# Kernel optimization log

Hardware: AMD Instinct MI355X
Metric: run time of the kernel (lower is better)

Reference implementation:

```python
import jax, jax.numpy as jnp
import numpy as np

DIM_IN, DIM_Q, DIM_K = 1024, 128, 128
B, S = 8, 2048

def setup_inputs() -> dict:
    key = jax.random.key(0)
    ks = jax.random.split(key, 9)
    sq = 1.0 / np.sqrt(DIM_IN)
    return {
        "query": jax.random.normal(ks[0], (B, S, DIM_IN), jnp.float32),
        "key": jax.random.normal(ks[1], (B, S, DIM_IN), jnp.float32),
        "value": jax.random.normal(ks[2], (B, S, DIM_IN), jnp.float32),
        "Wq": jax.random.uniform(ks[3], (DIM_IN, DIM_Q), jnp.float32, -sq, sq),
        "bq": jax.random.uniform(ks[4], (DIM_Q,), jnp.float32, -sq, sq),
        "Wk": jax.random.uniform(ks[5], (DIM_IN, DIM_K), jnp.float32, -sq, sq),
        "bk": jax.random.uniform(ks[6], (DIM_K,), jnp.float32, -sq, sq),
        "Wv": jax.random.uniform(ks[7], (DIM_IN, DIM_K), jnp.float32, -sq, sq),
        "bv": jax.random.uniform(ks[8], (DIM_K,), jnp.float32, -sq, sq),
    }

def reference(query, key, value, Wq, bq, Wk, bk, Wv, bv):
    q = jnp.einsum("bsd,dq->bsq", query, Wq) + bq          # [B,S,Dq]
    k = jnp.einsum("bsd,dk->bsk", key, Wk) + bk            # [B,S,Dk]
    v = jnp.einsum("bsd,dk->bsk", value, Wv) + bv          # [B,S,Dk]
    scale = jnp.asarray(q.shape[-1] ** 0.5, q.dtype)
    scores = jnp.einsum("bqd,bkd->bqk", q, k) / scale      # [B,S,S]
    attn = jax.nn.softmax(scores, axis=-1)
    return jnp.einsum("bqk,bkd->bqd", attn, v)             # [B,S,Dk]
```

## Files before the change

### kernel.cpp

```cpp
#include <hip/hip_runtime.h>

typedef __attribute__((ext_vector_type(8))) short short8;
typedef __attribute__((ext_vector_type(4))) float floatx4;

#define MFMA16(a, b, c) __builtin_amdgcn_mfma_f32_16x16x32_bf16(a, b, c, 0, 0, 0)

__device__ __forceinline__ short f2bf(float f) {
    unsigned int u = __float_as_uint(f);
    u = u + 0x7fffu + ((u >> 16) & 1u);
    return (short)(u >> 16);
}

__device__ __forceinline__ void ldst16(const void* g, void* l) {
    __builtin_amdgcn_global_load_lds(
        (const __attribute__((address_space(1))) void*)g,
        (__attribute__((address_space(3))) void*)l, 16, 0, 0);
}

__global__ __launch_bounds__(256) void wconv_kernel(const float* __restrict__ Wq,
                                                    const float* __restrict__ Wk,
                                                    const float* __restrict__ Wv,
                                                    short* __restrict__ wt) {
    int idx = blockIdx.x * 256 + threadIdx.x;
    int w = idx >> 17;
    int rem = idx & 131071;
    int k = rem >> 7, n = rem & 127;
    const float* W = (w == 0) ? Wq : (w == 1) ? Wk : Wv;
    wt[w * 131072 + n * 1024 + k] = f2bf(W[rem]);
}

__global__ __launch_bounds__(128, 3) void proj_kernel(const float* __restrict__ Q,
                                                      const float* __restrict__ K,
                                                      const float* __restrict__ V,
                                                      const short* __restrict__ wt,
                                                      const float* __restrict__ bq,
                                                      const float* __restrict__ bk,
                                                      const float* __restrict__ bv,
                                                      short* __restrict__ qo,
                                                      short* __restrict__ ko,
                                                      short* __restrict__ vo) {
    alignas(16) __shared__ float Asl[32 * 64];
    alignas(16) __shared__ short Wsl[128 * 64];
    const int t = threadIdx.x;
    const int wv = t >> 6, L = t & 63;
    const int q4 = L >> 4, l16 = L & 15;
    const int which = blockIdx.y;
    const float* A = (which == 0) ? Q : (which == 1) ? K : V;
    const short* Wt = wt + which * 131072;
    const float* bias = (which == 0) ? bq : (which == 1) ? bk : bv;
    const int m0 = blockIdx.x * 32;
    const int mw = m0 + 16 * wv;

    floatx4 acc[8];
    for (int nt = 0; nt < 8; nt++) acc[nt] = (floatx4)0.0f;

    for (int k0 = 0; k0 < 1024; k0 += 64) {
        __syncthreads();
        for (int j = 0; j < 4; j++) {
            int s = j * 128 + t;
            int r = s >> 4, c = (s & 15) ^ (r & 15);
            ldst16(A + (size_t)(m0 + r) * 1024 + k0 + c * 4,
                   Asl + (j * 128 + 64 * wv) * 4);
        }
        for (int j = 0; j < 8; j++) {
            int s = j * 128 + t;
            int r = s >> 3, c = (s & 7) ^ (r & 7);
            ldst16(Wt + (size_t)r * 1024 + k0 + c * 8,
                   Wsl + (j * 128 + 64 * wv) * 8);
        }
        __syncthreads();

        for (int ks = 0; ks < 2; ks++) {
            int c0 = 8 * ks + 2 * q4;
            const int ar = 16 * wv + l16;
            float4 f0 = *(float4*)&Asl[ar * 64 + (c0 ^ l16) * 4];
            float4 f1 = *(float4*)&Asl[ar * 64 + ((c0 + 1) ^ l16) * 4];
            short8 af;
            af[0] = f2bf(f0.x); af[1] = f2bf(f0.y); af[2] = f2bf(f0.z); af[3] = f2bf(f0.w);
            af[4] = f2bf(f1.x); af[5] = f2bf(f1.y); af[6] = f2bf(f1.z); af[7] = f2bf(f1.w);
            int cw = 4 * ks + q4;
            for (int nt = 0; nt < 8; nt++) {
                int wr = 16 * nt + l16;
                short8 bf = *(short8*)&Wsl[wr * 64 + (cw ^ (l16 & 7)) * 8];
                acc[nt] = MFMA16(af, bf, acc[nt]);
            }
        }
    }

    for (int nt = 0; nt < 8; nt++) {
        float bvv = bias[16 * nt + l16];
        for (int r = 0; r < 4; r++) {
            float val = acc[nt][r] + bvv;
            short h = f2bf(val);
            int grow = mw + q4 * 4 + r;
            int col = 16 * nt + l16;
            if (which == 0) {
                qo[(size_t)grow * 128 + col] = h;
            } else if (which == 1) {
                ko[(size_t)grow * 128 + col] = h;
            } else {
                int bb = grow >> 11, s = grow & 2047;
                vo[(size_t)bb * 262144 + (size_t)col * 2048 + s] = h;
            }
        }
    }
}

__global__ __launch_bounds__(512, 2) void flash_kernel(const short* __restrict__ qw,
                                                       const short* __restrict__ kw,
                                                       const short* __restrict__ vw,
                                                       float* __restrict__ out) {
    alignas(16) __shared__ short Kls[2][64 * 128];
    alignas(16) __shared__ short Vls[2][128 * 64];
    alignas(16) __shared__ short Pl[2][64][72];
    const int t = threadIdx.x;
    const int wvi = t >> 6, L = t & 63;
    const int pr = wvi >> 2, wq = wvi & 3;
    const int pt = t & 255;
    const int q4 = L >> 4, l16 = L & 15;
    const int bq = blockIdx.x, b = blockIdx.y;
    const short* qp = qw + (size_t)b * 262144 + (size_t)bq * 64 * 128;
    const short* kp = kw + (size_t)b * 262144;
    const short* vp = vw + (size_t)b * 262144;

    short8 qf[4];
    for (int ks = 0; ks < 4; ks++)
        qf[ks] = *(const short8*)(qp + (16 * wq + l16) * 128 + ks * 32 + q4 * 8);

    floatx4 oacc[8];
    for (int dt = 0; dt < 8; dt++) oacc[dt] = (floatx4)0.0f;
    float ps[4] = {0.f, 0.f, 0.f, 0.f};
    const float SL = (float)(0.08838834764831845 * 1.4426950408889634);

    for (int kt = 0; kt < 16; kt++) {
        const int kv0 = pr * 1024 + kt * 64;
        __syncthreads();
        for (int j = 0; j < 4; j++) {
            int s = j * 256 + pt;
            int r = s >> 4, c = (s & 15) ^ (r & 15);
            ldst16(kp + (size_t)(kv0 + r) * 128 + c * 8,
                   &Kls[pr][(j * 256 + 64 * wq) * 8]);
        }
        for (int j = 0; j < 4; j++) {
            int s = j * 256 + pt;
            int r = s >> 3, c = (s & 7) ^ (r & 7);
            ldst16(vp + (size_t)r * 2048 + kv0 + c * 8,
                   &Vls[pr][(j * 256 + 64 * wq) * 8]);
        }
        __syncthreads();

        floatx4 sa[4];
        for (int nt = 0; nt < 4; nt++) {
            sa[nt] = (floatx4)0.0f;
            for (int ks = 0; ks < 4; ks++) {
                short8 bfr = *(short8*)&Kls[pr][(16 * nt + l16) * 128 + ((4 * ks + q4) ^ l16) * 8];
                sa[nt] = MFMA16(qf[ks], bfr, sa[nt]);
            }
        }

        for (int nt = 0; nt < 4; nt++) {
            for (int r = 0; r < 4; r++) {
                float pv = __builtin_amdgcn_exp2f(sa[nt][r] * SL - 4.0f);
                ps[r] += pv;
                Pl[pr][16 * wq + q4 * 4 + r][16 * nt + l16] = f2bf(pv);
            }
        }

        short8 pf0 = *(short8*)&Pl[pr][16 * wq + l16][q4 * 8];
        short8 pf1 = *(short8*)&Pl[pr][16 * wq + l16][32 + q4 * 8];
        for (int dt = 0; dt < 8; dt++) {
            short8 v0 = *(short8*)&Vls[pr][(16 * dt + l16) * 64 + (q4 ^ (l16 & 7)) * 8];
            short8 v1 = *(short8*)&Vls[pr][(16 * dt + l16) * 64 + ((4 + q4) ^ (l16 & 7)) * 8];
            oacc[dt] = MFMA16(pf0, v0, oacc[dt]);
            oacc[dt] = MFMA16(pf1, v1, oacc[dt]);
        }
    }

    for (int r = 0; r < 4; r++)
        for (int off = 1; off <= 8; off <<= 1)
            ps[r] += __shfl_xor(ps[r], off, 64);

    __syncthreads();
    float* Om = (float*)&Kls[0][0];
    float* Lm = (float*)&Vls[0][0];
    if (pr == 1) {
        for (int dt = 0; dt < 8; dt++)
            for (int r = 0; r < 4; r++)
                Om[(16 * wq + q4 * 4 + r) * 128 + 16 * dt + l16] = oacc[dt][r];
        if (l16 == 0)
            for (int r = 0; r < 4; r++)
                Lm[16 * wq + q4 * 4 + r] = ps[r];
    }
    __syncthreads();
    if (pr == 0) {
        float inv[4];
        for (int r = 0; r < 4; r++)
            inv[r] = 1.0f / (ps[r] + Lm[16 * wq + q4 * 4 + r]);
        for (int dt = 0; dt < 8; dt++) {
            for (int r = 0; r < 4; r++) {
                int row = 16 * wq + q4 * 4 + r;
                int qrow = bq * 64 + row;
                out[((size_t)b * 2048 + qrow) * 128 + 16 * dt + l16] =
                    (oacc[dt][r] + Om[row * 128 + 16 * dt + l16]) * inv[r];
            }
        }
    }
}

extern "C" void kernel_launch(void* const* d_in, const int* in_sizes, int n_in,
                              void* d_out, int out_size, void* d_ws, size_t ws_size,
                              hipStream_t stream) {
    const float* query = (const float*)d_in[0];
    const float* key   = (const float*)d_in[1];
    const float* value = (const float*)d_in[2];
    const float* Wq    = (const float*)d_in[3];
    const float* bq    = (const float*)d_in[4];
    const float* Wk    = (const float*)d_in[5];
    const float* bk    = (const float*)d_in[6];
    const float* Wv    = (const float*)d_in[7];
    const float* bv    = (const float*)d_in[8];
    float* out = (float*)d_out;

    short* wt  = (short*)d_ws;
    short* qws = wt + 3 * 131072;
    short* kws = qws + 16384 * 128;
    short* vws = kws + 16384 * 128;

    wconv_kernel<<<1536, 256, 0, stream>>>(Wq, Wk, Wv, wt);
    proj_kernel<<<dim3(512, 3), 128, 0, stream>>>(query, key, value, wt,
                                                  bq, bk, bv, qws, kws, vws);
    flash_kernel<<<dim3(32, 8), 512, 0, stream>>>(qws, kws, vws, out);
}
```

Baseline: 271.3 us.

## Drop LDS staging in projection; load A and W directly into registers with prefetch

```diff
diff --git a/kernel.cpp b/kernel.cpp
--- a/kernel.cpp
+++ b/kernel.cpp
@@ -29,18 +29,16 @@
     wt[w * 131072 + n * 1024 + k] = f2bf(W[rem]);
 }
 
-__global__ __launch_bounds__(128, 3) void proj_kernel(const float* __restrict__ Q,
-                                                      const float* __restrict__ K,
-                                                      const float* __restrict__ V,
-                                                      const short* __restrict__ wt,
-                                                      const float* __restrict__ bq,
-                                                      const float* __restrict__ bk,
-                                                      const float* __restrict__ bv,
-                                                      short* __restrict__ qo,
-                                                      short* __restrict__ ko,
-                                                      short* __restrict__ vo) {
-    alignas(16) __shared__ float Asl[32 * 64];
-    alignas(16) __shared__ short Wsl[128 * 64];
+__global__ __launch_bounds__(128) void proj_kernel(const float* __restrict__ Q,
+                                                   const float* __restrict__ K,
+                                                   const float* __restrict__ V,
+                                                   const short* __restrict__ wt,
+                                                   const float* __restrict__ bq,
+                                                   const float* __restrict__ bk,
+                                                   const float* __restrict__ bv,
+                                                   short* __restrict__ qo,
+                                                   short* __restrict__ ko,
+                                                   short* __restrict__ vo) {
     const int t = threadIdx.x;
     const int wv = t >> 6, L = t & 63;
     const int q4 = L >> 4, l16 = L & 15;
@@ -48,59 +46,81 @@
     const float* A = (which == 0) ? Q : (which == 1) ? K : V;
     const short* Wt = wt + which * 131072;
     const float* bias = (which == 0) ? bq : (which == 1) ? bk : bv;
-    const int m0 = blockIdx.x * 32;
-    const int mw = m0 + 16 * wv;
-
-    floatx4 acc[8];
-    for (int nt = 0; nt < 8; nt++) acc[nt] = (floatx4)0.0f;
+    const int m0 = blockIdx.x * 64 + wv * 32;
+
+    floatx4 acc[2][8];
+#pragma unroll
+    for (int rg = 0; rg < 2; rg++)
+#pragma unroll
+        for (int nt = 0; nt < 8; nt++) acc[rg][nt] = (floatx4)0.0f;
+
+    const float* a0 = A + (size_t)(m0 + l16) * 1024 + 8 * q4;
+    const float* a1 = a0 + 16 * 1024;
+    const short* wb = Wt + (size_t)l16 * 1024 + 8 * q4;
+
+    float4 pa[2][2][2];
+#pragma unroll
+    for (int rg = 0; rg < 2; rg++) {
+        const float* ap = rg ? a1 : a0;
+#pragma unroll
+        for (int ks = 0; ks < 2; ks++) {
+            pa[rg][ks][0] = *(const float4*)(ap + 32 * ks);
+            pa[rg][ks][1] = *(const float4*)(ap + 32 * ks + 4);
+        }
+    }
 
     for (int k0 = 0; k0 < 1024; k0 += 64) {
-        __syncthreads();
-        for (int j = 0; j < 4; j++) {
-            int s = j * 128 + t;
-            int r = s >> 4, c = (s & 15) ^ (r & 15);
-            ldst16(A + (size_t)(m0 + r) * 1024 + k0 + c * 4,
-                   Asl + (j * 128 + 64 * wv) * 4);
-        }
-        for (int j = 0; j < 8; j++) {
-            int s = j * 128 + t;
-            int r = s >> 3, c = (s & 7) ^ (r & 7);
-            ldst16(Wt + (size_t)r * 1024 + k0 + c * 8,
-                   Wsl + (j * 128 + 64 * wv) * 8);
-        }
-        __syncthreads();
-
-        for (int ks = 0; ks < 2; ks++) {
-            int c0 = 8 * ks + 2 * q4;
-            const int ar = 16 * wv + l16;
-            float4 f0 = *(float4*)&Asl[ar * 64 + (c0 ^ l16) * 4];
-            float4 f1 = *(float4*)&Asl[ar * 64 + ((c0 + 1) ^ l16) * 4];
-            short8 af;
-            af[0] = f2bf(f0.x); af[1] = f2bf(f0.y); af[2] = f2bf(f0.z); af[3] = f2bf(f0.w);
-            af[4] = f2bf(f1.x); af[5] = f2bf(f1.y); af[6] = f2bf(f1.z); af[7] = f2bf(f1.w);
-            int cw = 4 * ks + q4;
+        short8 af[2][2];
+#pragma unroll
+        for (int rg = 0; rg < 2; rg++)
+#pragma unroll
+            for (int ks = 0; ks < 2; ks++) {
+                float4 f0 = pa[rg][ks][0], f1 = pa[rg][ks][1];
+                short8 v;
+                v[0] = f2bf(f0.x); v[1] = f2bf(f0.y); v[2] = f2bf(f0.z); v[3] = f2bf(f0.w);
+                v[4] = f2bf(f1.x); v[5] = f2bf(f1.y); v[6] = f2bf(f1.z); v[7] = f2bf(f1.w);
+                af[rg][ks] = v;
+            }
+        if (k0 + 64 < 1024) {
+#pragma unroll
+            for (int rg = 0; rg < 2; rg++) {
+                const float* ap = (rg ? a1 : a0) + k0 + 64;
+#pragma unroll
+                for (int ks = 0; ks < 2; ks++) {
+                    pa[rg][ks][0] = *(const float4*)(ap + 32 * ks);
+                    pa[rg][ks][1] = *(const float4*)(ap + 32 * ks + 4);
+                }
+            }
+        }
+#pragma unroll
+        for (int ks = 0; ks < 2; ks++)
+#pragma unroll
             for (int nt = 0; nt < 8; nt++) {
-                int wr = 16 * nt + l16;
-                short8 bf = *(short8*)&Wsl[wr * 64 + (cw ^ (l16 & 7)) * 8];
-                acc[nt] = MFMA16(af, bf, acc[nt]);
-            }
-        }
-    }
-
-    for (int nt = 0; nt < 8; nt++) {
-        float bvv = bias[16 * nt + l16];
-        for (int r = 0; r < 4; r++) {
-            float val = acc[nt][r] + bvv;
-            short h = f2bf(val);
-            int grow = mw + q4 * 4 + r;
-            int col = 16 * nt + l16;
-            if (which == 0) {
-                qo[(size_t)grow * 128 + col] = h;
-            } else if (which == 1) {
-                ko[(size_t)grow * 128 + col] = h;
-            } else {
-                int bb = grow >> 11, s = grow & 2047;
-                vo[(size_t)bb * 262144 + (size_t)col * 2048 + s] = h;
+                short8 bf = *(const short8*)(wb + (size_t)nt * 16384 + k0 + 32 * ks);
+                acc[0][nt] = MFMA16(af[0][ks], bf, acc[0][nt]);
+                acc[1][nt] = MFMA16(af[1][ks], bf, acc[1][nt]);
+            }
+    }
+
+#pragma unroll
+    for (int rg = 0; rg < 2; rg++) {
+        const int rbase = m0 + rg * 16 + q4 * 4;
+#pragma unroll
+        for (int nt = 0; nt < 8; nt++) {
+            const int col = 16 * nt + l16;
+            float bvv = bias[col];
+#pragma unroll
+            for (int r = 0; r < 4; r++) {
+                short h = f2bf(acc[rg][nt][r] + bvv);
+                int grow = rbase + r;
+                if (which == 0) {
+                    qo[(size_t)grow * 128 + col] = h;
+                } else if (which == 1) {
+                    ko[(size_t)grow * 128 + col] = h;
+                } else {
+                    int bb = grow >> 11, s = grow & 2047;
+                    vo[(size_t)bb * 262144 + (size_t)col * 2048 + s] = h;
+                }
             }
         }
     }
@@ -227,7 +247,7 @@
     short* vws = kws + 16384 * 128;
 
     wconv_kernel<<<1536, 256, 0, stream>>>(Wq, Wk, Wv, wt);
-    proj_kernel<<<dim3(512, 3), 128, 0, stream>>>(query, key, value, wt,
+    proj_kernel<<<dim3(256, 3), 128, 0, stream>>>(query, key, value, wt,
                                                   bq, bk, bv, qws, kws, vws);
     flash_kernel<<<dim3(32, 8), 512, 0, stream>>>(qws, kws, vws, out);
 }
```

After: 282.0 us. 4.0% more time.

## Register-prefetch projection without LDS and double-buffer K/V tiles in flash kernel

Applied to the files above, without the earlier changes.

```diff
diff --git a/kernel.cpp b/kernel.cpp
--- a/kernel.cpp
+++ b/kernel.cpp
@@ -29,7 +29,36 @@
     wt[w * 131072 + n * 1024 + k] = f2bf(W[rem]);
 }
 
-__global__ __launch_bounds__(128, 3) void proj_kernel(const float* __restrict__ Q,
+#define CONV8(dst, f0, f1)                                                  \
+    {                                                                       \
+        dst[0] = f2bf(f0.x); dst[1] = f2bf(f0.y);                           \
+        dst[2] = f2bf(f0.z); dst[3] = f2bf(f0.w);                           \
+        dst[4] = f2bf(f1.x); dst[5] = f2bf(f1.y);                           \
+        dst[6] = f2bf(f1.z); dst[7] = f2bf(f1.w);                           \
+    }
+
+#define SUBSTEP(P0, P1, P2, P3, cc)                                         \
+    {                                                                       \
+        short8 af0, af1;                                                    \
+        CONV8(af0, P0, P1);                                                 \
+        CONV8(af1, P2, P3);                                                 \
+        if ((cc) + 2 < 16) {                                                \
+            const float* ap = aP + ((cc) + 2) * 64;                         \
+            P0 = *(const float4*)(ap);                                      \
+            P1 = *(const float4*)(ap + 4);                                  \
+            P2 = *(const float4*)(ap + 32);                                 \
+            P3 = *(const float4*)(ap + 36);                                 \
+        }                                                                   \
+        _Pragma("unroll")                                                   \
+        for (int nt = 0; nt < 4; nt++) {                                    \
+            short8 b0 = *(const short8*)(wP + nt * 16384 + (cc) * 64);      \
+            short8 b1 = *(const short8*)(wP + nt * 16384 + (cc) * 64 + 32); \
+            acc[nt] = MFMA16(af0, b0, acc[nt]);                             \
+            acc[nt] = MFMA16(af1, b1, acc[nt]);                             \
+        }                                                                   \
+    }
+
+__global__ __launch_bounds__(128, 4) void proj_kernel(const float* __restrict__ Q,
                                                       const float* __restrict__ K,
                                                       const float* __restrict__ V,
                                                       const short* __restrict__ wt,
@@ -39,8 +68,6 @@
                                                       short* __restrict__ qo,
                                                       short* __restrict__ ko,
                                                       short* __restrict__ vo) {
-    alignas(16) __shared__ float Asl[32 * 64];
-    alignas(16) __shared__ short Wsl[128 * 64];
     const int t = threadIdx.x;
     const int wv = t >> 6, L = t & 63;
     const int q4 = L >> 4, l16 = L & 15;
@@ -48,52 +75,39 @@
     const float* A = (which == 0) ? Q : (which == 1) ? K : V;
     const short* Wt = wt + which * 131072;
     const float* bias = (which == 0) ? bq : (which == 1) ? bk : bv;
-    const int m0 = blockIdx.x * 32;
-    const int mw = m0 + 16 * wv;
-
-    floatx4 acc[8];
-    for (int nt = 0; nt < 8; nt++) acc[nt] = (floatx4)0.0f;
-
-    for (int k0 = 0; k0 < 1024; k0 += 64) {
-        __syncthreads();
-        for (int j = 0; j < 4; j++) {
-            int s = j * 128 + t;
-            int r = s >> 4, c = (s & 15) ^ (r & 15);
-            ldst16(A + (size_t)(m0 + r) * 1024 + k0 + c * 4,
-                   Asl + (j * 128 + 64 * wv) * 4);
-        }
-        for (int j = 0; j < 8; j++) {
-            int s = j * 128 + t;
-            int r = s >> 3, c = (s & 7) ^ (r & 7);
-            ldst16(Wt + (size_t)r * 1024 + k0 + c * 8,
-                   Wsl + (j * 128 + 64 * wv) * 8);
-        }
-        __syncthreads();
-
-        for (int ks = 0; ks < 2; ks++) {
-            int c0 = 8 * ks + 2 * q4;
-            const int ar = 16 * wv + l16;
-            float4 f0 = *(float4*)&Asl[ar * 64 + (c0 ^ l16) * 4];
-            float4 f1 = *(float4*)&Asl[ar * 64 + ((c0 + 1) ^ l16) * 4];
-            short8 af;
-            af[0] = f2bf(f0.x); af[1] = f2bf(f0.y); af[2] = f2bf(f0.z); af[3] = f2bf(f0.w);
-            af[4] = f2bf(f1.x); af[5] = f2bf(f1.y); af[6] = f2bf(f1.z); af[7] = f2bf(f1.w);
-            int cw = 4 * ks + q4;
-            for (int nt = 0; nt < 8; nt++) {
-                int wr = 16 * nt + l16;
-                short8 bf = *(short8*)&Wsl[wr * 64 + (cw ^ (l16 & 7)) * 8];
-                acc[nt] = MFMA16(af, bf, acc[nt]);
-            }
-        }
-    }
-
-    for (int nt = 0; nt < 8; nt++) {
-        float bvv = bias[16 * nt + l16];
+    const int m0 = blockIdx.x * 16;
+    const int n0 = wv * 64;
+
+    floatx4 acc[4];
+#pragma unroll
+    for (int nt = 0; nt < 4; nt++) acc[nt] = (floatx4)0.0f;
+
+    const float* aP = A + (size_t)(m0 + l16) * 1024 + 8 * q4;
+    const short* wP = Wt + (size_t)(n0 + l16) * 1024 + 8 * q4;
+
+    float4 pA0 = *(const float4*)(aP);
+    float4 pA1 = *(const float4*)(aP + 4);
+    float4 pA2 = *(const float4*)(aP + 32);
+    float4 pA3 = *(const float4*)(aP + 36);
+    float4 pB0 = *(const float4*)(aP + 64);
+    float4 pB1 = *(const float4*)(aP + 68);
+    float4 pB2 = *(const float4*)(aP + 96);
+    float4 pB3 = *(const float4*)(aP + 100);
+
+    for (int c = 0; c < 16; c += 2) {
+        SUBSTEP(pA0, pA1, pA2, pA3, c);
+        SUBSTEP(pB0, pB1, pB2, pB3, c + 1);
+    }
+
+    const int rbase = m0 + q4 * 4;
+#pragma unroll
+    for (int nt = 0; nt < 4; nt++) {
+        const int col = n0 + 16 * nt + l16;
+        float bvv = bias[col];
+#pragma unroll
         for (int r = 0; r < 4; r++) {
-            float val = acc[nt][r] + bvv;
-            short h = f2bf(val);
-            int grow = mw + q4 * 4 + r;
-            int col = 16 * nt + l16;
+            short h = f2bf(acc[nt][r] + bvv);
+            int grow = rbase + r;
             if (which == 0) {
                 qo[(size_t)grow * 128 + col] = h;
             } else if (which == 1) {
@@ -110,8 +124,8 @@
                                                        const short* __restrict__ kw,
                                                        const short* __restrict__ vw,
                                                        float* __restrict__ out) {
-    alignas(16) __shared__ short Kls[2][64 * 128];
-    alignas(16) __shared__ short Vls[2][128 * 64];
+    alignas(16) __shared__ short Kls[2][2][64 * 128];
+    alignas(16) __shared__ short Vls[2][2][128 * 64];
     alignas(16) __shared__ short Pl[2][64][72];
     const int t = threadIdx.x;
     const int wvi = t >> 6, L = t & 63;
@@ -132,28 +146,34 @@
     float ps[4] = {0.f, 0.f, 0.f, 0.f};
     const float SL = (float)(0.08838834764831845 * 1.4426950408889634);
 
-    for (int kt = 0; kt < 16; kt++) {
+    auto stage = [&](int buf, int kt) {
         const int kv0 = pr * 1024 + kt * 64;
-        __syncthreads();
         for (int j = 0; j < 4; j++) {
             int s = j * 256 + pt;
             int r = s >> 4, c = (s & 15) ^ (r & 15);
             ldst16(kp + (size_t)(kv0 + r) * 128 + c * 8,
-                   &Kls[pr][(j * 256 + 64 * wq) * 8]);
+                   &Kls[buf][pr][(j * 256 + 64 * wq) * 8]);
         }
         for (int j = 0; j < 4; j++) {
             int s = j * 256 + pt;
             int r = s >> 3, c = (s & 7) ^ (r & 7);
             ldst16(vp + (size_t)r * 2048 + kv0 + c * 8,
-                   &Vls[pr][(j * 256 + 64 * wq) * 8]);
-        }
+                   &Vls[buf][pr][(j * 256 + 64 * wq) * 8]);
+        }
+    };
+
+    stage(0, 0);
+
+    for (int kt = 0; kt < 16; kt++) {
+        const int cur = kt & 1;
         __syncthreads();
+        if (kt + 1 < 16) stage(cur ^ 1, kt + 1);
 
         floatx4 sa[4];
         for (int nt = 0; nt < 4; nt++) {
             sa[nt] = (floatx4)0.0f;
             for (int ks = 0; ks < 4; ks++) {
-                short8 bfr = *(short8*)&Kls[pr][(16 * nt + l16) * 128 + ((4 * ks + q4) ^ l16) * 8];
+                short8 bfr = *(short8*)&Kls[cur][pr][(16 * nt + l16) * 128 + ((4 * ks + q4) ^ l16) * 8];
                 sa[nt] = MFMA16(qf[ks], bfr, sa[nt]);
             }
         }
@@ -169,8 +189,8 @@
         short8 pf0 = *(short8*)&Pl[pr][16 * wq + l16][q4 * 8];
         short8 pf1 = *(short8*)&Pl[pr][16 * wq + l16][32 + q4 * 8];
         for (int dt = 0; dt < 8; dt++) {
-            short8 v0 = *(short8*)&Vls[pr][(16 * dt + l16) * 64 + (q4 ^ (l16 & 7)) * 8];
-            short8 v1 = *(short8*)&Vls[pr][(16 * dt + l16) * 64 + ((4 + q4) ^ (l16 & 7)) * 8];
+            short8 v0 = *(short8*)&Vls[cur][pr][(16 * dt + l16) * 64 + (q4 ^ (l16 & 7)) * 8];
+            short8 v1 = *(short8*)&Vls[cur][pr][(16 * dt + l16) * 64 + ((4 + q4) ^ (l16 & 7)) * 8];
             oacc[dt] = MFMA16(pf0, v0, oacc[dt]);
             oacc[dt] = MFMA16(pf1, v1, oacc[dt]);
         }
@@ -181,8 +201,8 @@
             ps[r] += __shfl_xor(ps[r], off, 64);
 
     __syncthreads();
-    float* Om = (float*)&Kls[0][0];
-    float* Lm = (float*)&Vls[0][0];
+    float* Om = (float*)&Kls[0][0][0];
+    float* Lm = (float*)&Vls[0][0][0];
     if (pr == 1) {
         for (int dt = 0; dt < 8; dt++)
             for (int r = 0; r < 4; r++)
@@ -227,7 +247,7 @@
     short* vws = kws + 16384 * 128;
 
     wconv_kernel<<<1536, 256, 0, stream>>>(Wq, Wk, Wv, wt);
-    proj_kernel<<<dim3(512, 3), 128, 0, stream>>>(query, key, value, wt,
-                                                  bq, bk, bv, qws, kws, vws);
+    proj_kernel<<<dim3(1024, 3), 128, 0, stream>>>(query, key, value, wt,
+                                                   bq, bk, bv, qws, kws, vws);
     flash_kernel<<<dim3(32, 8), 512, 0, stream>>>(qws, kws, vws, out);
 }
```

Result: slower. 328.8 us (+21.2%).
